# Kernel optimization log

Measured on AMD Instinct MI355X. Metric: run time of the kernel, lower is better.

## Reference

```python
import jax, jax.numpy as jnp
import numpy as np

B, S, H = 4, 2048, 1536
NH, HD = 12, 128          # num_heads, head_dim
K = 4                     # base_kernel
INNER = 4 * H             # GLU inner dim
EPS = 1e-6
CONV_DILS = (1, 2, 4, 8, 16, 32)
HEAD_DILS = [(1, 2, 4), (1, 1, 1), (4, 8, 16), (8, 16, 32), (32, 64, 128),
             (64, 128, 256), (256, 512, 1024), (1, 100, 200), (1, 500, 1000),
             (1, 1024, 2048), (3, 9, 27), (5, 25, 125)]


def setup_inputs() -> dict:
    key = jax.random.key(0)
    ks = jax.random.split(key, 20)
    sd = 0.02
    inp = {
        'x': jax.random.normal(ks[0], (B, S, H), dtype=jnp.float32),
        'norm_w': jnp.ones((3, H), dtype=jnp.float32),
        # DilatedConvStack: 6 depthwise convs (C=H, K=4) + proj Linear(H,H)
        'conv_ws': jax.random.normal(ks[1], (6, H, 1, K), dtype=jnp.float32) * sd,
        'conv_bs': jax.random.normal(ks[2], (6, H), dtype=jnp.float32) * sd,
        'conv_proj_w': jax.random.normal(ks[3], (H, H), dtype=jnp.float32) * sd,
        'conv_proj_b': jax.random.normal(ks[4], (H,), dtype=jnp.float32) * sd,
        # MultiHeadDilatedState
        'gate_w': jax.random.normal(ks[5], (2 * H, H), dtype=jnp.float32) * sd,
        'router_w': jax.random.normal(ks[6], (NH, H), dtype=jnp.float32) * sd,
        'router_b': jax.random.normal(ks[7], (NH,), dtype=jnp.float32) * sd,
        'head_ws': jax.random.normal(ks[8], (NH, 3, HD, 1, K), dtype=jnp.float32) * sd,
        'head_bs': jax.random.normal(ks[9], (NH, 3, HD), dtype=jnp.float32) * sd,
        'mix_gate_w': jax.random.normal(ks[10], (H, H), dtype=jnp.float32) * sd,
        'mix_gate_b': jnp.full((H,), 2.0, dtype=jnp.float32),
        'mixing_w': jax.random.normal(ks[11], (H, H), dtype=jnp.float32) * sd,
        'mixing_b': jax.random.normal(ks[12], (H,), dtype=jnp.float32) * sd,
        # GLU FFN
        'ffn_in_w': jax.random.normal(ks[13], (2 * INNER, H), dtype=jnp.float32) * sd,
        'ffn_out_w': jax.random.normal(ks[14], (H, INNER), dtype=jnp.float32) * sd,
        # path gates (Linear(H,1) x 3)
        'pg_w': jax.random.normal(ks[15], (3, H), dtype=jnp.float32) * sd,
        'pg_b': jnp.full((3,), 2.0, dtype=jnp.float32),
    }
    return inp


def rmsnorm(x, w):
    norm = jax.lax.rsqrt(jnp.mean(x * x, axis=-1, keepdims=True) + EPS)
    return x * norm * w


def dconv(h, w, b, d):
    # h: [B, C, S], w: [C, 1, K] depthwise, causal left-pad (K-1)*d
    C = h.shape[1]
    pad = (K - 1) * d
    y = jax.lax.conv_general_dilated(
        h, w, window_strides=(1,), padding=[(pad, 0)], rhs_dilation=(d,),
        dimension_numbers=('NCH', 'OIH', 'NCH'), feature_group_count=C)
    return y + b[None, :, None]


def reference(x, norm_w, conv_ws, conv_bs, conv_proj_w, conv_proj_b,
              gate_w, router_w, router_b, head_ws, head_bs,
              mix_gate_w, mix_gate_b, mixing_w, mixing_b,
              ffn_in_w, ffn_out_w, pg_w, pg_b):
    n1 = rmsnorm(x, norm_w[0])
    n2 = rmsnorm(x, norm_w[1])
    n3 = rmsnorm(x, norm_w[2])
    gc = jax.nn.sigmoid(jnp.einsum('bsh,h->bs', n1, pg_w[0]) + pg_b[0])[..., None]
    gs = jax.nn.sigmoid(jnp.einsum('bsh,h->bs', n2, pg_w[1]) + pg_b[1])[..., None]
    gf = jax.nn.sigmoid(jnp.einsum('bsh,h->bs', n3, pg_w[2]) + pg_b[2])[..., None]

    # --- DilatedConvStack path ---
    h = jnp.swapaxes(n1, 1, 2)  # [B, H, S]
    for i, d in enumerate(CONV_DILS):
        h = h + jax.nn.gelu(dconv(h, conv_ws[i], conv_bs[i], d), approximate=False)
    conv_out = jnp.swapaxes(h, 1, 2) @ conv_proj_w.T + conv_proj_b
    x = x + gc * conv_out

    # --- MultiHeadDilatedState path ---
    head_weights = jax.nn.sigmoid(n2 @ router_w.T + router_b)  # [B, S, NH]
    g = n2 @ gate_w.T                                          # [B, S, 2H]
    content, gate = jnp.split(g, 2, axis=-1)
    x_gated = content * jax.nn.sigmoid(gate)
    x_heads = x_gated.reshape(B, S, NH, HD)
    outs = []
    for i in range(NH):
        hh = jnp.swapaxes(x_heads[:, :, i, :], 1, 2)  # [B, HD, S]
        for j, d in enumerate(HEAD_DILS[i]):
            hh = hh + dconv(hh, head_ws[i, j], head_bs[i, j], d)
        hh = jnp.swapaxes(hh, 1, 2)                   # [B, S, HD]
        outs.append(hh * head_weights[:, :, i:i + 1])
    out = jnp.concatenate(outs, axis=-1)              # [B, S, H]
    out = out * jax.nn.sigmoid(out @ mix_gate_w.T + mix_gate_b)
    state_out = out @ mixing_w.T + mixing_b
    x = x + gs * state_out

    # --- GLU FFN path ---
    hff = n3 @ ffn_in_w.T
    c, gt = jnp.split(hff, 2, axis=-1)
    ffn_out = (c * jax.nn.sigmoid(gt)) @ ffn_out_w.T
    x = x + gf * ffn_out
    return x
```

## Files before the change

### kernel.cpp

```cpp
#include <hip/hip_runtime.h>
#include <stdint.h>

#define H 1536
#define SQ 2048
#define BB 4
#define MT 8192
#define NHD 12
#define INNER 6144
#define EPSF 1e-6f

typedef unsigned short u16;
typedef __bf16 b16x8 __attribute__((ext_vector_type(8)));
typedef float f32x4 __attribute__((ext_vector_type(4)));

__device__ __forceinline__ u16 f2b(float f) {
  uint32_t u = __float_as_uint(f);
  u = u + 0x7fffu + ((u >> 16) & 1u);
  return (u16)(u >> 16);
}
__device__ __forceinline__ float b2f(u16 u) { return __uint_as_float(((uint32_t)u) << 16); }
__device__ __forceinline__ float sigm(float x) { return 1.0f / (1.0f + __expf(-x)); }
__device__ __forceinline__ float gelu_exact(float x) {
  return 0.5f * x * (1.0f + erff(x * 0.70710678118654752f));
}
__device__ __forceinline__ void load_lds16(const void* g, void* l) {
  __builtin_amdgcn_global_load_lds(
      (__attribute__((address_space(1))) void*)(g),
      (__attribute__((address_space(3))) void*)(l), 16, 0, 0);
}

__global__ __launch_bounds__(256) void k_rmsnorm(const float* __restrict__ x, u16* __restrict__ xb) {
  int m = blockIdx.x, t = threadIdx.x;
  const float* row = x + (size_t)m * H;
  float v[6]; float ss = 0.f;
#pragma unroll
  for (int j = 0; j < 6; ++j) { v[j] = row[t + j * 256]; ss += v[j] * v[j]; }
#pragma unroll
  for (int o = 32; o > 0; o >>= 1) ss += __shfl_xor(ss, o);
  __shared__ float red[4];
  if ((t & 63) == 0) red[t >> 6] = ss;
  __syncthreads();
  float r = rsqrtf((red[0] + red[1] + red[2] + red[3]) / (float)H + EPSF);
#pragma unroll
  for (int j = 0; j < 6; ++j) xb[(size_t)m * H + t + j * 256] = f2b(v[j] * r);
}

__global__ __launch_bounds__(256) void k_gates(const u16* __restrict__ xb, const float* __restrict__ norm_w,
    const float* __restrict__ pg_w, const float* __restrict__ pg_b,
    const float* __restrict__ router_w, const float* __restrict__ router_b,
    float* __restrict__ gates, float* __restrict__ hw) {
  int m = blockIdx.x, t = threadIdx.x;
  const u16* row = xb + (size_t)m * H;
  float acc[15];
#pragma unroll
  for (int i = 0; i < 15; ++i) acc[i] = 0.f;
  for (int j = 0; j < 6; ++j) {
    int c = t + j * 256;
    float xv = b2f(row[c]);
    float n0 = norm_w[c], n1 = norm_w[H + c], n2 = norm_w[2 * H + c];
    acc[0] += xv * n0 * pg_w[c];
    acc[1] += xv * n1 * pg_w[H + c];
    acc[2] += xv * n2 * pg_w[2 * H + c];
    float xn = xv * n1;
#pragma unroll
    for (int i = 0; i < 12; ++i) acc[3 + i] += xn * router_w[(size_t)i * H + c];
  }
  __shared__ float red[15][4];
#pragma unroll
  for (int i = 0; i < 15; ++i) {
    float s = acc[i];
#pragma unroll
    for (int o = 32; o > 0; o >>= 1) s += __shfl_xor(s, o);
    if ((t & 63) == 0) red[i][t >> 6] = s;
  }
  __syncthreads();
  if (t < 15) {
    float s = red[t][0] + red[t][1] + red[t][2] + red[t][3];
    if (t < 3) gates[t * MT + m] = sigm(s + pg_b[t]);
    else hw[(size_t)m * NHD + (t - 3)] = sigm(s + router_b[t - 3]);
  }
}

__global__ __launch_bounds__(256) void k_wcvt(const float* __restrict__ w, u16* __restrict__ wb,
                                              const float* __restrict__ cs, int K) {
  int c = blockIdx.x * 256 + threadIdx.x;
  size_t r = blockIdx.y;
  float v = w[r * K + c];
  if (cs) v *= cs[c];
  wb[r * K + c] = f2b(v);
}
__global__ __launch_bounds__(256) void k_wcvt2(const float* __restrict__ w, u16* __restrict__ wb,
                                               const float* __restrict__ cs, int K, int HALF) {
  int c = blockIdx.x * 256 + threadIdx.x;
  int rr = blockIdx.y;
  int src = (rr & 1) ? (HALF + (rr >> 1)) : (rr >> 1);
  wb[(size_t)rr * K + c] = f2b(w[(size_t)src * K + c] * cs[c]);
}

__global__ __launch_bounds__(256) void k_conv(const u16* __restrict__ in, u16* __restrict__ out,
    const float* __restrict__ w, const float* __restrict__ bias, int d, const float* __restrict__ insc) {
  int c = blockIdx.x * 256 + threadIdx.x;
  int s = blockIdx.y, b = blockIdx.z;
  float sc = insc ? insc[c] : 1.f;
  const u16* base = in + (size_t)b * SQ * H + c;
  float4 wv = *(const float4*)(w + (size_t)c * 4);
  float center = b2f(base[(size_t)s * H]) * sc;
  float acc = bias[c] + wv.w * center;
  if (s - d     >= 0) acc += wv.z * b2f(base[(size_t)(s - d) * H]) * sc;
  if (s - 2 * d >= 0) acc += wv.y * b2f(base[(size_t)(s - 2 * d) * H]) * sc;
  if (s - 3 * d >= 0) acc += wv.x * b2f(base[(size_t)(s - 3 * d) * H]) * sc;
  out[((size_t)b * SQ + s) * H + c] = f2b(center + gelu_exact(acc));
}

__constant__ int HDILS[36] = {1,2,4, 1,1,1, 4,8,16, 8,16,32, 32,64,128, 64,128,256,
                              256,512,1024, 1,100,200, 1,500,1000, 1,1024,2048, 3,9,27, 5,25,125};

__global__ __launch_bounds__(256) void k_hconv(const u16* __restrict__ in, u16* __restrict__ out,
    const float* __restrict__ hws, const float* __restrict__ hbs, int j) {
  int c = blockIdx.x * 256 + threadIdx.x;
  int s = blockIdx.y, b = blockIdx.z;
  int head = c >> 7, cc = c & 127;
  int d = HDILS[head * 3 + j];
  size_t wi = (size_t)(head * 3 + j) * 128 + cc;
  float4 wv = *(const float4*)(hws + wi * 4);
  const u16* base = in + (size_t)b * SQ * H + c;
  float center = b2f(base[(size_t)s * H]);
  float acc = hbs[wi] + wv.w * center;
  if (s - d     >= 0) acc += wv.z * b2f(base[(size_t)(s - d) * H]);
  if (s - 2 * d >= 0) acc += wv.y * b2f(base[(size_t)(s - 2 * d) * H]);
  if (s - 3 * d >= 0) acc += wv.x * b2f(base[(size_t)(s - 3 * d) * H]);
  out[((size_t)b * SQ + s) * H + c] = f2b(center + acc);
}

__global__ __launch_bounds__(256) void k_headout(const u16* __restrict__ in, const float* __restrict__ hw,
                                                 u16* __restrict__ ob) {
  int c = blockIdx.x * 256 + threadIdx.x;
  size_t m = blockIdx.y;
  ob[m * H + c] = f2b(b2f(in[m * H + c]) * hw[m * NHD + (c >> 7)]);
}

__global__ __launch_bounds__(256) void k_final(const float* __restrict__ x, float* __restrict__ out, size_t n) {
  size_t i = (size_t)blockIdx.x * 256 + threadIdx.x, st = (size_t)gridDim.x * 256;
  for (; i < n; i += st) out[i] = x[i] + out[i];
}

#define MMQ(AF, BF, MO, NO)                                                      \
  _Pragma("unroll") for (int m_ = 0; m_ < 4; ++m_)                               \
  _Pragma("unroll") for (int n_ = 0; n_ < 2; ++n_)                               \
  _Pragma("unroll") for (int ks_ = 0; ks_ < 2; ++ks_)                            \
    acc[(MO) + m_][(NO) + n_] = __builtin_amdgcn_mfma_f32_16x16x32_bf16(         \
        AF[m_][ks_], BF[n_][ks_], acc[(MO) + m_][(NO) + n_], 0, 0, 0);

#define TILE(BUF, SKO, DOSTAGE, VMSTMT)                                          \
  {                                                                              \
    b16x8 alo[4][2], ahi[4][2], blo[2][2], bhi[2][2];                            \
    _Pragma("unroll") for (int m = 0; m < 4; ++m) {                              \
      alo[m][0] = *(const b16x8*)(Ard0 + (BUF) * 16384 + m * 1024);              \
      alo[m][1] = *(const b16x8*)(Ard1 + (BUF) * 16384 + m * 1024);              \
    }                                                                            \
    _Pragma("unroll") for (int n = 0; n < 2; ++n) {                              \
      blo[n][0] = *(const b16x8*)(Brd0 + (BUF) * 16384 + n * 1024);              \
      blo[n][1] = *(const b16x8*)(Brd1 + (BUF) * 16384 + n * 1024);              \
    }                                                                            \
    asm volatile("s_waitcnt lgkmcnt(8)" ::: "memory");                           \
    __builtin_amdgcn_sched_barrier(0);                                           \
    __builtin_amdgcn_s_barrier();                                                \
    asm volatile("s_waitcnt lgkmcnt(0)" ::: "memory");                           \
    __builtin_amdgcn_sched_barrier(0);                                           \
    __builtin_amdgcn_s_setprio(1);                                               \
    MMQ(alo, blo, 0, 0);                                                         \
    __builtin_amdgcn_s_setprio(0);                                               \
    __builtin_amdgcn_sched_barrier(0);                                           \
    __builtin_amdgcn_s_barrier();                                                \
    _Pragma("unroll") for (int n = 0; n < 2; ++n) {                              \
      bhi[n][0] = *(const b16x8*)(Brd0 + (BUF) * 16384 + 2048 + n * 1024);       \
      bhi[n][1] = *(const b16x8*)(Brd1 + (BUF) * 16384 + 2048 + n * 1024);       \
    }                                                                            \
    __builtin_amdgcn_sched_barrier(0);                                           \
    __builtin_amdgcn_s_barrier();                                                \
    asm volatile("s_waitcnt lgkmcnt(0)" ::: "memory");                           \
    __builtin_amdgcn_sched_barrier(0);                                           \
    __builtin_amdgcn_s_setprio(1);                                               \
    MMQ(alo, bhi, 0, 2);                                                         \
    __builtin_amdgcn_s_setprio(0);                                               \
    __builtin_amdgcn_sched_barrier(0);                                           \
    __builtin_amdgcn_s_barrier();                                                \
    _Pragma("unroll") for (int m = 0; m < 4; ++m) {                              \
      ahi[m][0] = *(const b16x8*)(Ard0 + (BUF) * 16384 + 4096 + m * 1024);       \
      ahi[m][1] = *(const b16x8*)(Ard1 + (BUF) * 16384 + 4096 + m * 1024);       \
    }                                                                            \
    if (DOSTAGE) {                                                               \
      load_lds16(Bg + (boff0 + (SKO)), dB0 + (BUF) * 16384);                     \
      load_lds16(Bg + (boff1 + (SKO)), dB1 + (BUF) * 16384);                     \
      load_lds16(Bg + (boff2 + (SKO)), dB2 + (BUF) * 16384);                     \
      load_lds16(Bg + (boff3 + (SKO)), dB3 + (BUF) * 16384);                     \
    }                                                                            \
    __builtin_amdgcn_sched_barrier(0);                                           \
    __builtin_amdgcn_s_barrier();                                                \
    asm volatile("s_waitcnt lgkmcnt(0)" ::: "memory");                           \
    __builtin_amdgcn_sched_barrier(0);                                           \
    __builtin_amdgcn_s_setprio(1);                                               \
    MMQ(ahi, bhi, 4, 2);                                                         \
    __builtin_amdgcn_s_setprio(0);                                               \
    __builtin_amdgcn_sched_barrier(0);                                           \
    __builtin_amdgcn_s_barrier();                                                \
    if (DOSTAGE) {                                                               \
      load_lds16(Ag + (aoff0 + (SKO)), dA0 + (BUF) * 16384);                     \
      load_lds16(Ag + (aoff1 + (SKO)), dA1 + (BUF) * 16384);                     \
      load_lds16(Ag + (aoff2 + (SKO)), dA2 + (BUF) * 16384);                     \
      load_lds16(Ag + (aoff3 + (SKO)), dA3 + (BUF) * 16384);                     \
    }                                                                            \
    __builtin_amdgcn_sched_barrier(0);                                           \
    __builtin_amdgcn_s_barrier();                                                \
    __builtin_amdgcn_s_setprio(1);                                               \
    MMQ(ahi, blo, 4, 0);                                                         \
    __builtin_amdgcn_s_setprio(0);                                               \
    VMSTMT;                                                                      \
    __builtin_amdgcn_sched_barrier(0);                                           \
    __builtin_amdgcn_s_barrier();                                                \
  }

template<int MODE>
__global__ __launch_bounds__(512, 2) void k_gemm(const u16* __restrict__ A, int lda,
    const u16* __restrict__ B, int ldb, void* __restrict__ Cout, int M, int N, int K,
    const float* __restrict__ bias, const float* __restrict__ gate, const u16* __restrict__ aux) {
  __shared__ u16 lds[65536];
  int tid = threadIdx.x;
  int w = tid >> 6, lane = tid & 63;
  int l15 = lane & 15, l4 = lane >> 4;
  int wr = w >> 2, wc = w & 3;

  int gx = gridDim.x, gy = gridDim.y;
  int nwg = gx * gy;
  int bid = blockIdx.y * gx + blockIdx.x;
  int bm, bn;
  if (((nwg & 7) == 0) && ((gy & 7) == 0)) {
    int xcd = bid & 7, l = bid >> 3;
    int rpx = gy >> 3;
    bm = xcd * rpx + (l % rpx);
    bn = l / rpx;
  } else { bn = bid % gx; bm = bid / gx; }

  const u16* Ag = A + (size_t)bm * 256 * lda;
  const u16* Bg = B + (size_t)bn * 256 * ldb;
  int nt = K >> 6;

  f32x4 acc[8][4];
#pragma unroll
  for (int m = 0; m < 8; ++m)
#pragma unroll
    for (int n = 0; n < 4; ++n) acc[m][n] = f32x4{0.f, 0.f, 0.f, 0.f};

  int m7 = l15 & 7;
  int slot0 = l4 ^ m7, slot1 = slot0 ^ 4;
  u16* Ard0 = lds + wr * 8192 + l15 * 64 + slot0 * 8;
  u16* Ard1 = lds + wr * 8192 + l15 * 64 + slot1 * 8;
  u16* Brd0 = lds + 32768 + (wc >> 1) * 8192 + ((wc & 1) * 64 + l15) * 64 + slot0 * 8;
  u16* Brd1 = lds + 32768 + (wc >> 1) * 8192 + ((wc & 1) * 64 + l15) * 64 + slot1 * 8;

  int r0 = tid >> 3;
  int kg = ((lane & 7) ^ (lane >> 3)) * 8;
  int aoff0 = (0 * 128 + 0 * 64 + r0) * lda + kg;
  int aoff1 = (0 * 128 + 1 * 64 + r0) * lda + kg;
  int aoff2 = (1 * 128 + 0 * 64 + r0) * lda + kg;
  int aoff3 = (1 * 128 + 1 * 64 + r0) * lda + kg;
  int boff0 = (0 * 128 + 0 * 64 + r0) * ldb + kg;
  int boff1 = (0 * 128 + 1 * 64 + r0) * ldb + kg;
  int boff2 = (1 * 128 + 0 * 64 + r0) * ldb + kg;
  int boff3 = (1 * 128 + 1 * 64 + r0) * ldb + kg;
  int w512 = w * 512;
  u16* dA0 = lds + 0 * 8192 + 0 * 4096 + w512;
  u16* dA1 = lds + 0 * 8192 + 1 * 4096 + w512;
  u16* dA2 = lds + 1 * 8192 + 0 * 4096 + w512;
  u16* dA3 = lds + 1 * 8192 + 1 * 4096 + w512;
  u16* dB0 = lds + 32768 + 0 * 8192 + 0 * 4096 + w512;
  u16* dB1 = lds + 32768 + 1 * 4096 + w512;
  u16* dB2 = lds + 32768 + 8192 + w512;
  u16* dB3 = lds + 32768 + 8192 + 4096 + w512;

  load_lds16(Bg + boff0, dB0); load_lds16(Bg + boff1, dB1);
  load_lds16(Bg + boff2, dB2); load_lds16(Bg + boff3, dB3);
  load_lds16(Ag + aoff0, dA0); load_lds16(Ag + aoff1, dA1);
  load_lds16(Ag + aoff2, dA2); load_lds16(Ag + aoff3, dA3);
  load_lds16(Bg + boff0 + 64, dB0 + 16384); load_lds16(Bg + boff1 + 64, dB1 + 16384);
  load_lds16(Bg + boff2 + 64, dB2 + 16384); load_lds16(Bg + boff3 + 64, dB3 + 16384);
  load_lds16(Ag + aoff0 + 64, dA0 + 16384); load_lds16(Ag + aoff1 + 64, dA1 + 16384);
  load_lds16(Ag + aoff2 + 64, dA2 + 16384); load_lds16(Ag + aoff3 + 64, dA3 + 16384);
  asm volatile("s_waitcnt vmcnt(8)" ::: "memory");
  __builtin_amdgcn_s_barrier();
  __builtin_amdgcn_sched_barrier(0);

  int koff = 0;
  int main_iters = (nt >> 1) - 1;
  for (int it = 0; it < main_iters; ++it) {
    TILE(0, koff + 128, true, asm volatile("s_waitcnt vmcnt(8)" ::: "memory"));
    TILE(1, koff + 192, true, asm volatile("s_waitcnt vmcnt(8)" ::: "memory"));
    koff += 128;
  }
  TILE(0, 0, false, asm volatile("s_waitcnt vmcnt(0)" ::: "memory"));
  TILE(1, 0, false, (void)0);

  int rowbase = bm * 256 + wr * 128;
  int colbase = bn * 256 + wc * 64;
#pragma unroll
  for (int n = 0; n < 4; ++n) {
    int col = colbase + n * 16 + l15;
    float bv = (MODE == 2) ? 0.f : (bias ? bias[col] : 0.f);
#pragma unroll
    for (int m = 0; m < 8; ++m) {
#pragma unroll
      for (int j = 0; j < 4; ++j) {
        int r = rowbase + m * 16 + l4 * 4 + j;
        float val = acc[m][n][j];
        if (MODE == 0) {
          ((float*)Cout)[(size_t)r * N + col] = (val + bv) * gate[r];
        } else if (MODE == 1) {
          ((float*)Cout)[(size_t)r * N + col] += (val + bv) * (gate ? gate[r] : 1.f);
        } else if (MODE == 2) {
          float other = __shfl_xor(val, 1);
          if ((lane & 1) == 0)
            ((u16*)Cout)[(size_t)r * (N >> 1) + (col >> 1)] = f2b(val * sigm(other));
        } else {
          float a = b2f(aux[(size_t)r * N + col]);
          ((u16*)Cout)[(size_t)r * N + col] = f2b(a * sigm(val + bv));
        }
      }
    }
  }
}

extern "C" void kernel_launch(void* const* d_in, const int* in_sizes, int n_in,
                              void* d_out, int out_size, void* d_ws, size_t ws_size,
                              hipStream_t stream) {
  const float* x        = (const float*)d_in[0];
  const float* norm_w   = (const float*)d_in[1];
  const float* conv_ws  = (const float*)d_in[2];
  const float* conv_bs  = (const float*)d_in[3];
  const float* conv_pw  = (const float*)d_in[4];
  const float* conv_pb  = (const float*)d_in[5];
  const float* gate_w   = (const float*)d_in[6];
  const float* router_w = (const float*)d_in[7];
  const float* router_b = (const float*)d_in[8];
  const float* head_ws  = (const float*)d_in[9];
  const float* head_bs  = (const float*)d_in[10];
  const float* mixg_w   = (const float*)d_in[11];
  const float* mixg_b   = (const float*)d_in[12];
  const float* mix_w    = (const float*)d_in[13];
  const float* mix_b    = (const float*)d_in[14];
  const float* ffn_iw   = (const float*)d_in[15];
  const float* ffn_ow   = (const float*)d_in[16];
  const float* pg_w     = (const float*)d_in[17];
  const float* pg_b     = (const float*)d_in[18];
  float* out = (float*)d_out;

  char* ws = (char*)d_ws;
  size_t o = 0;
  auto alloc = [&](size_t n) { char* p = ws + o; o += n; return p; };
  u16*  XB  = (u16*)alloc(25165824);
  u16*  A16 = (u16*)alloc(25165824);
  u16*  B16 = (u16*)alloc(25165824);
  u16*  WG2 = (u16*)alloc(9437184);
  u16*  WP  = (u16*)alloc(4718592);
  u16*  WMG = (u16*)alloc(4718592);
  u16*  WMX = (u16*)alloc(4718592);
  u16*  WFI = (u16*)alloc(37748736);
  u16*  WFO = (u16*)alloc(18874368);
  float* gates = (float*)alloc(98304);
  float* hw    = (float*)alloc(393216);
  u16*  VB = A16;

  k_rmsnorm<<<MT, 256, 0, stream>>>(x, XB);
  k_gates<<<MT, 256, 0, stream>>>(XB, norm_w, pg_w, pg_b, router_w, router_b, gates, hw);

  k_wcvt2<<<dim3(6, 3072),  256, 0, stream>>>(gate_w, WG2, norm_w + H, H, H);
  k_wcvt <<<dim3(6, 1536),  256, 0, stream>>>(conv_pw, WP, nullptr, H);
  k_wcvt <<<dim3(6, 1536),  256, 0, stream>>>(mixg_w, WMG, nullptr, H);
  k_wcvt <<<dim3(6, 1536),  256, 0, stream>>>(mix_w, WMX, nullptr, H);
  k_wcvt2<<<dim3(6, 12288), 256, 0, stream>>>(ffn_iw, WFI, norm_w + 2 * H, H, INNER);
  k_wcvt <<<dim3(24, 1536), 256, 0, stream>>>(ffn_ow, WFO, nullptr, INNER);

  dim3 cg(6, SQ, BB);
  k_conv<<<cg, 256, 0, stream>>>(XB,  A16, conv_ws + 0 * H * 4, conv_bs + 0 * H, 1,  norm_w);
  k_conv<<<cg, 256, 0, stream>>>(A16, B16, conv_ws + 1 * H * 4, conv_bs + 1 * H, 2,  nullptr);
  k_conv<<<cg, 256, 0, stream>>>(B16, A16, conv_ws + 2 * H * 4, conv_bs + 2 * H, 4,  nullptr);
  k_conv<<<cg, 256, 0, stream>>>(A16, B16, conv_ws + 3 * H * 4, conv_bs + 3 * H, 8,  nullptr);
  k_conv<<<cg, 256, 0, stream>>>(B16, A16, conv_ws + 4 * H * 4, conv_bs + 4 * H, 16, nullptr);
  k_conv<<<cg, 256, 0, stream>>>(A16, B16, conv_ws + 5 * H * 4, conv_bs + 5 * H, 32, nullptr);
  k_gemm<0><<<dim3(6, 32), 512, 0, stream>>>(B16, H, WP, H, out, MT, H, H, conv_pb, gates, nullptr);

  k_gemm<2><<<dim3(12, 32), 512, 0, stream>>>(XB, H, WG2, H, A16, MT, 2 * H, H, nullptr, nullptr, nullptr);
  k_hconv<<<cg, 256, 0, stream>>>(A16, B16, head_ws, head_bs, 0);
  k_hconv<<<cg, 256, 0, stream>>>(B16, A16, head_ws, head_bs, 1);
  k_hconv<<<cg, 256, 0, stream>>>(A16, B16, head_ws, head_bs, 2);
  k_headout<<<dim3(6, MT), 256, 0, stream>>>(B16, hw, A16);
  k_gemm<3><<<dim3(6, 32), 512, 0, stream>>>(A16, H, WMG, H, B16, MT, H, H, mixg_b, nullptr, A16);
  k_gemm<1><<<dim3(6, 32), 512, 0, stream>>>(B16, H, WMX, H, out, MT, H, H, mix_b, gates + MT, nullptr);

  for (int ch = 0; ch < 2; ++ch) {
    k_gemm<2><<<dim3(24, 32), 512, 0, stream>>>(XB, H, WFI + (size_t)ch * 6144 * H, H,
                                                VB, MT, 6144, H, nullptr, nullptr, nullptr);
    k_gemm<1><<<dim3(6, 32), 512, 0, stream>>>(VB, 3072, WFO + ch * 3072, INNER,
                                               out, MT, H, 3072, nullptr, gates + 2 * MT, nullptr);
  }

  k_final<<<2048, 256, 0, stream>>>(x, out, (size_t)MT * H);
}
```

Measured before the change: 1.446 ms.

## Restructure GEMM main loop to prefetch next tile's LDS fragments across barriers

Rewrites the double-buffered bf16 MFMA GEMM tile macro so each tile loads the next buffer's low A/B fragments into registers while the current tile's later MFMA quadrants run. The number of workgroup barriers per tile drops from about six to two, and all global-to-LDS staging for a tile is issued at once after the first barrier. The goal is to hide LDS read latency and cut barrier stalls. In exchange it doubles the fragment register sets, which raises VGPR pressure and can lower occupancy.

Measured after the change: 2.022 ms. 1.4x slower.

```diff
diff --git a/kernel.cpp b/kernel.cpp
--- a/kernel.cpp
+++ b/kernel.cpp
@@ -151,73 +151,63 @@
     acc[(MO) + m_][(NO) + n_] = __builtin_amdgcn_mfma_f32_16x16x32_bf16(         \
         AF[m_][ks_], BF[n_][ks_], acc[(MO) + m_][(NO) + n_], 0, 0, 0);
 
-#define TILE(BUF, SKO, DOSTAGE, VMSTMT)                                          \
+#define TILE(ALOC, BLOC, ALON, BLON, AHIC, BHIC, BOFF, NBOFF, SKO, DOST, DORD, DOMID) \
   {                                                                              \
-    b16x8 alo[4][2], ahi[4][2], blo[2][2], bhi[2][2];                            \
+    asm volatile("s_waitcnt lgkmcnt(0)" ::: "memory");                           \
+    __builtin_amdgcn_sched_barrier(0);                                           \
+    _Pragma("unroll") for (int n = 0; n < 2; ++n) {                              \
+      BHIC[n][0] = *(const b16x8*)(Brd0 + (BOFF) + 2048 + n * 1024);             \
+      BHIC[n][1] = *(const b16x8*)(Brd1 + (BOFF) + 2048 + n * 1024);             \
+    }                                                                            \
     _Pragma("unroll") for (int m = 0; m < 4; ++m) {                              \
-      alo[m][0] = *(const b16x8*)(Ard0 + (BUF) * 16384 + m * 1024);              \
-      alo[m][1] = *(const b16x8*)(Ard1 + (BUF) * 16384 + m * 1024);              \
+      AHIC[m][0] = *(const b16x8*)(Ard0 + (BOFF) + 4096 + m * 1024);             \
+      AHIC[m][1] = *(const b16x8*)(Ard1 + (BOFF) + 4096 + m * 1024);             \
     }                                                                            \
-    _Pragma("unroll") for (int n = 0; n < 2; ++n) {                              \
-      blo[n][0] = *(const b16x8*)(Brd0 + (BUF) * 16384 + n * 1024);              \
-      blo[n][1] = *(const b16x8*)(Brd1 + (BUF) * 16384 + n * 1024);              \
+    __builtin_amdgcn_sched_barrier(0);                                           \
+    __builtin_amdgcn_s_setprio(1);                                               \
+    MMQ(ALOC, BLOC, 0, 0);                                                       \
+    __builtin_amdgcn_s_setprio(0);                                               \
+    asm volatile("s_waitcnt lgkmcnt(0)" ::: "memory");                           \
+    __builtin_amdgcn_sched_barrier(0);                                           \
+    __builtin_amdgcn_s_barrier();                                                \
+    __builtin_amdgcn_sched_barrier(0);                                           \
+    if (DOST) {                                                                  \
+      load_lds16(Bg + (boff0 + (SKO)), dB0 + (BOFF));                            \
+      load_lds16(Bg + (boff1 + (SKO)), dB1 + (BOFF));                            \
+      load_lds16(Bg + (boff2 + (SKO)), dB2 + (BOFF));                            \
+      load_lds16(Bg + (boff3 + (SKO)), dB3 + (BOFF));                            \
+      load_lds16(Ag + (aoff0 + (SKO)), dA0 + (BOFF));                            \
+      load_lds16(Ag + (aoff1 + (SKO)), dA1 + (BOFF));                            \
+      load_lds16(Ag + (aoff2 + (SKO)), dA2 + (BOFF));                            \
+      load_lds16(Ag + (aoff3 + (SKO)), dA3 + (BOFF));                            \
     }                                                                            \
-    asm volatile("s_waitcnt lgkmcnt(8)" ::: "memory");                           \
-    __builtin_amdgcn_sched_barrier(0);                                           \
-    __builtin_amdgcn_s_barrier();                                                \
-    asm volatile("s_waitcnt lgkmcnt(0)" ::: "memory");                           \
     __builtin_amdgcn_sched_barrier(0);                                           \
     __builtin_amdgcn_s_setprio(1);                                               \
-    MMQ(alo, blo, 0, 0);                                                         \
+    MMQ(ALOC, BHIC, 0, 2);                                                       \
     __builtin_amdgcn_s_setprio(0);                                               \
-    __builtin_amdgcn_sched_barrier(0);                                           \
-    __builtin_amdgcn_s_barrier();                                                \
-    _Pragma("unroll") for (int n = 0; n < 2; ++n) {                              \
-      bhi[n][0] = *(const b16x8*)(Brd0 + (BUF) * 16384 + 2048 + n * 1024);       \
-      bhi[n][1] = *(const b16x8*)(Brd1 + (BUF) * 16384 + 2048 + n * 1024);       \
+    if ((DOMID) == 1) { asm volatile("s_waitcnt vmcnt(8)" ::: "memory"); }       \
+    else if ((DOMID) == 2) { asm volatile("s_waitcnt vmcnt(0)" ::: "memory"); }  \
+    if (DOMID) {                                                                 \
+      __builtin_amdgcn_sched_barrier(0);                                         \
+      __builtin_amdgcn_s_barrier();                                              \
+      __builtin_amdgcn_sched_barrier(0);                                         \
     }                                                                            \
-    __builtin_amdgcn_sched_barrier(0);                                           \
-    __builtin_amdgcn_s_barrier();                                                \
-    asm volatile("s_waitcnt lgkmcnt(0)" ::: "memory");                           \
+    if (DORD) {                                                                  \
+      _Pragma("unroll") for (int m = 0; m < 4; ++m) {                            \
+        ALON[m][0] = *(const b16x8*)(Ard0 + (NBOFF) + m * 1024);                 \
+        ALON[m][1] = *(const b16x8*)(Ard1 + (NBOFF) + m * 1024);                 \
+      }                                                                          \
+      _Pragma("unroll") for (int n = 0; n < 2; ++n) {                            \
+        BLON[n][0] = *(const b16x8*)(Brd0 + (NBOFF) + n * 1024);                 \
+        BLON[n][1] = *(const b16x8*)(Brd1 + (NBOFF) + n * 1024);                 \
+      }                                                                          \
+    }                                                                            \
     __builtin_amdgcn_sched_barrier(0);                                           \
     __builtin_amdgcn_s_setprio(1);                                               \
-    MMQ(alo, bhi, 0, 2);                                                         \
+    MMQ(AHIC, BHIC, 4, 2);                                                       \
+    MMQ(AHIC, BLOC, 4, 0);                                                       \
     __builtin_amdgcn_s_setprio(0);                                               \
     __builtin_amdgcn_sched_barrier(0);                                           \
-    __builtin_amdgcn_s_barrier();                                                \
-    _Pragma("unroll") for (int m = 0; m < 4; ++m) {                              \
-      ahi[m][0] = *(const b16x8*)(Ard0 + (BUF) * 16384 + 4096 + m * 1024);       \
-      ahi[m][1] = *(const b16x8*)(Ard1 + (BUF) * 16384 + 4096 + m * 1024);       \
-    }                                                                            \
-    if (DOSTAGE) {                                                               \
-      load_lds16(Bg + (boff0 + (SKO)), dB0 + (BUF) * 16384);                     \
-      load_lds16(Bg + (boff1 + (SKO)), dB1 + (BUF) * 16384);                     \
-      load_lds16(Bg + (boff2 + (SKO)), dB2 + (BUF) * 16384);                     \
-      load_lds16(Bg + (boff3 + (SKO)), dB3 + (BUF) * 16384);                     \
-    }                                                                            \
-    __builtin_amdgcn_sched_barrier(0);                                           \
-    __builtin_amdgcn_s_barrier();                                                \
-    asm volatile("s_waitcnt lgkmcnt(0)" ::: "memory");                           \
-    __builtin_amdgcn_sched_barrier(0);                                           \
-    __builtin_amdgcn_s_setprio(1);                                               \
-    MMQ(ahi, bhi, 4, 2);                                                         \
-    __builtin_amdgcn_s_setprio(0);                                               \
-    __builtin_amdgcn_sched_barrier(0);                                           \
-    __builtin_amdgcn_s_barrier();                                                \
-    if (DOSTAGE) {                                                               \
-      load_lds16(Ag + (aoff0 + (SKO)), dA0 + (BUF) * 16384);                     \
-      load_lds16(Ag + (aoff1 + (SKO)), dA1 + (BUF) * 16384);                     \
-      load_lds16(Ag + (aoff2 + (SKO)), dA2 + (BUF) * 16384);                     \
-      load_lds16(Ag + (aoff3 + (SKO)), dA3 + (BUF) * 16384);                     \
-    }                                                                            \
-    __builtin_amdgcn_sched_barrier(0);                                           \
-    __builtin_amdgcn_s_barrier();                                                \
-    __builtin_amdgcn_s_setprio(1);                                               \
-    MMQ(ahi, blo, 4, 0);                                                         \
-    __builtin_amdgcn_s_setprio(0);                                               \
-    VMSTMT;                                                                      \
-    __builtin_amdgcn_sched_barrier(0);                                           \
-    __builtin_amdgcn_s_barrier();                                                \
   }
 
 template<int MODE>
@@ -253,10 +243,10 @@
 
   int m7 = l15 & 7;
   int slot0 = l4 ^ m7, slot1 = slot0 ^ 4;
-  u16* Ard0 = lds + wr * 8192 + l15 * 64 + slot0 * 8;
-  u16* Ard1 = lds + wr * 8192 + l15 * 64 + slot1 * 8;
-  u16* Brd0 = lds + 32768 + (wc >> 1) * 8192 + ((wc & 1) * 64 + l15) * 64 + slot0 * 8;
-  u16* Brd1 = lds + 32768 + (wc >> 1) * 8192 + ((wc & 1) * 64 + l15) * 64 + slot1 * 8;
+  const u16* Ard0 = lds + wr * 8192 + l15 * 64 + slot0 * 8;
+  const u16* Ard1 = lds + wr * 8192 + l15 * 64 + slot1 * 8;
+  const u16* Brd0 = lds + 32768 + (wc >> 1) * 8192 + ((wc & 1) * 64 + l15) * 64 + slot0 * 8;
+  const u16* Brd1 = lds + 32768 + (wc >> 1) * 8192 + ((wc & 1) * 64 + l15) * 64 + slot1 * 8;
 
   int r0 = tid >> 3;
   int kg = ((lane & 7) ^ (lane >> 3)) * 8;
@@ -269,14 +259,17 @@
   int boff2 = (1 * 128 + 0 * 64 + r0) * ldb + kg;
   int boff3 = (1 * 128 + 1 * 64 + r0) * ldb + kg;
   int w512 = w * 512;
-  u16* dA0 = lds + 0 * 8192 + 0 * 4096 + w512;
-  u16* dA1 = lds + 0 * 8192 + 1 * 4096 + w512;
-  u16* dA2 = lds + 1 * 8192 + 0 * 4096 + w512;
-  u16* dA3 = lds + 1 * 8192 + 1 * 4096 + w512;
-  u16* dB0 = lds + 32768 + 0 * 8192 + 0 * 4096 + w512;
+  u16* dA0 = lds + 0 * 4096 + w512;
+  u16* dA1 = lds + 1 * 4096 + w512;
+  u16* dA2 = lds + 2 * 4096 + w512;
+  u16* dA3 = lds + 3 * 4096 + w512;
+  u16* dB0 = lds + 32768 + 0 * 4096 + w512;
   u16* dB1 = lds + 32768 + 1 * 4096 + w512;
-  u16* dB2 = lds + 32768 + 8192 + w512;
-  u16* dB3 = lds + 32768 + 8192 + 4096 + w512;
+  u16* dB2 = lds + 32768 + 2 * 4096 + w512;
+  u16* dB3 = lds + 32768 + 3 * 4096 + w512;
+
+  b16x8 alo0[4][2], alo1[4][2], ahi0[4][2], ahi1[4][2];
+  b16x8 blo0[2][2], blo1[2][2], bhi0[2][2], bhi1[2][2];
 
   load_lds16(Bg + boff0, dB0); load_lds16(Bg + boff1, dB1);
   load_lds16(Bg + boff2, dB2); load_lds16(Bg + boff3, dB3);
@@ -287,18 +280,30 @@
   load_lds16(Ag + aoff0 + 64, dA0 + 16384); load_lds16(Ag + aoff1 + 64, dA1 + 16384);
   load_lds16(Ag + aoff2 + 64, dA2 + 16384); load_lds16(Ag + aoff3 + 64, dA3 + 16384);
   asm volatile("s_waitcnt vmcnt(8)" ::: "memory");
+  __builtin_amdgcn_sched_barrier(0);
   __builtin_amdgcn_s_barrier();
   __builtin_amdgcn_sched_barrier(0);
+#pragma unroll
+  for (int m = 0; m < 4; ++m) {
+    alo0[m][0] = *(const b16x8*)(Ard0 + m * 1024);
+    alo0[m][1] = *(const b16x8*)(Ard1 + m * 1024);
+  }
+#pragma unroll
+  for (int n = 0; n < 2; ++n) {
+    blo0[n][0] = *(const b16x8*)(Brd0 + n * 1024);
+    blo0[n][1] = *(const b16x8*)(Brd1 + n * 1024);
+  }
+  __builtin_amdgcn_sched_barrier(0);
 
   int koff = 0;
-  int main_iters = (nt >> 1) - 1;
-  for (int it = 0; it < main_iters; ++it) {
-    TILE(0, koff + 128, true, asm volatile("s_waitcnt vmcnt(8)" ::: "memory"));
-    TILE(1, koff + 192, true, asm volatile("s_waitcnt vmcnt(8)" ::: "memory"));
+  int pairs = nt >> 1;
+  for (int it = 0; it < pairs - 1; ++it) {
+    TILE(alo0, blo0, alo1, blo1, ahi0, bhi0, 0,     16384, koff + 128, 1, 1, 1);
+    TILE(alo1, blo1, alo0, blo0, ahi1, bhi1, 16384, 0,     koff + 192, 1, 1, 1);
     koff += 128;
   }
-  TILE(0, 0, false, asm volatile("s_waitcnt vmcnt(0)" ::: "memory"));
-  TILE(1, 0, false, (void)0);
+  TILE(alo0, blo0, alo1, blo1, ahi0, bhi0, 0,     16384, 0, 0, 1, 2);
+  TILE(alo1, blo1, alo0, blo0, ahi1, bhi1, 16384, 0,     0, 0, 0, 0);
 
   int rowbase = bm * 256 + wr * 128;
   int colbase = bn * 256 + wc * 64;
```
